# Performance work log

Hardware: AMD Instinct MI355X
Metric: run time of the kernel (lower is better)

Reference implementation:

```python
import jax, jax.numpy as jnp
import numpy as np

B, S, D, H, F, PD = 2, 2048, 768, 12, 3072, 64


def layer_norm(x, w, b, eps=1e-5):
    m = jnp.mean(x, axis=-1, keepdims=True)
    v = jnp.var(x, axis=-1, keepdims=True)
    return (x - m) / jnp.sqrt(v + eps) * w + b


def setup_inputs() -> dict:
    key = jax.random.key(0)
    ks = jax.random.split(key, 8)
    sc = 0.02
    return {
        "x": jax.random.normal(ks[0], (B, S, D), jnp.float32),
        "ln1_w": jnp.ones((D,), jnp.float32),
        "ln1_b": jnp.zeros((D,), jnp.float32),
        "in_proj_w": jax.random.normal(ks[1], (3 * D, D), jnp.float32) * sc,
        "in_proj_b": jnp.zeros((3 * D,), jnp.float32),
        "phase_w": jax.random.normal(ks[2], (PD, D), jnp.float32) * sc,
        "alpha": jnp.float32(0.5),
        "ff_w1": jax.random.normal(ks[3], (F, D), jnp.float32) * sc,
        "ff_b1": jnp.zeros((F,), jnp.float32),
        "ff_w2": jax.random.normal(ks[4], (D, F), jnp.float32) * sc,
        "ff_b2": jnp.zeros((D,), jnp.float32),
        "ln2_w": jnp.ones((D,), jnp.float32),
        "ln2_b": jnp.zeros((D,), jnp.float32),
    }


def reference(x, ln1_w, ln1_b, in_proj_w, in_proj_b, phase_w, alpha,
              ff_w1, ff_b1, ff_w2, ff_b2, ln2_w, ln2_b):
    Dh = D // H
    xn = layer_norm(x, ln1_w, ln1_b)
    # MultiheadAttention with need_weights=True: only the head-averaged
    # softmax(QK^T/sqrt(Dh)) weights are consumed downstream (attn_out is
    # discarded in the original forward, so V/out_proj are dead code).
    qkv = xn @ in_proj_w.T + in_proj_b                       # [B,S,3D]
    q, k, _ = jnp.split(qkv, 3, axis=-1)
    q = q.reshape(B, S, H, Dh) * (1.0 / np.sqrt(Dh)).astype(np.float32)
    k = k.reshape(B, S, H, Dh)
    scores = jnp.einsum('bqhd,bkhd->bhqk', q, k)             # [B,H,S,S]
    attn_w = jax.nn.softmax(scores, axis=-1).mean(axis=1)    # head-avg [B,S,S]
    phase = jnp.tanh(xn @ phase_w.T)                         # [B,S,64]
    phase_coh = (phase @ phase.swapaxes(-2, -1) + 1.0) * 0.5  # [B,S,S]
    blended = jax.nn.softmax(jnp.log(attn_w + 1e-6) + alpha * phase_coh, axis=-1)
    x = x + blended @ xn                                     # enhanced context
    x2 = layer_norm(x, ln2_w, ln2_b)
    h = jax.nn.gelu(x2 @ ff_w1.T + ff_b1, approximate=False)  # exact GELU (torch default)
    ff = h @ ff_w2.T + ff_b2
    return x + ff
```

## Files before the change

### kernel.cpp

```cpp
#include <hip/hip_runtime.h>
#include <math.h>

typedef unsigned short u16;
typedef short bf8 __attribute__((ext_vector_type(8)));
typedef float f4 __attribute__((ext_vector_type(4)));

#define LOG2E 1.44269504088896340736f

__device__ __forceinline__ u16 f2b(float f) {
  union { float f; unsigned int u; } v; v.f = f;
  unsigned int u = v.u;
  return (u16)((u + 0x7FFFu + ((u >> 16) & 1u)) >> 16);
}
__device__ __forceinline__ float b2f(u16 u) {
  union { unsigned int i; float f; } v; v.i = ((unsigned int)u) << 16; return v.f;
}
__device__ __forceinline__ float ex2(float x) {
#if __has_builtin(__builtin_amdgcn_exp2f)
  return __builtin_amdgcn_exp2f(x);
#else
  return exp2f(x);
#endif
}

template <int N>
__device__ __forceinline__ void waitvm() {
  if constexpr (N == 0)      asm volatile("s_waitcnt vmcnt(0)" ::: "memory");
  else if constexpr (N == 4) asm volatile("s_waitcnt vmcnt(4)" ::: "memory");
  else if constexpr (N == 6) asm volatile("s_waitcnt vmcnt(6)" ::: "memory");
  else if constexpr (N == 8) asm volatile("s_waitcnt vmcnt(8)" ::: "memory");
}

#define GLOAD_LDS16(gp, lp)                                                          \
  __builtin_amdgcn_global_load_lds(                                                  \
      reinterpret_cast<const __attribute__((address_space(1))) unsigned int*>(       \
          reinterpret_cast<uintptr_t>(gp)),                                          \
      reinterpret_cast<__attribute__((address_space(3))) unsigned int*>(             \
          reinterpret_cast<uintptr_t>(lp)),                                          \
      16, 0, 0)

template <int ISSUES>
__device__ __forceinline__ void stage_sw(const u16* gbase, long ldg, u16* lds,
                                         int wv, int lane) {
#pragma unroll
  for (int is = 0; is < ISSUES; ++is) {
    const int idx = is * 256 + wv * 64 + lane;
    const int r = idx >> 3, cs = idx & 7;
    const u16* gp = gbase + (long)r * ldg + ((cs ^ (r & 7)) << 3);
    GLOAD_LDS16(gp, (char*)lds + is * 4096 + wv * 1024);
  }
}
__device__ __forceinline__ bf8 frag_sw(const u16* lds, int r, int c) {
  return *(const bf8*)((const char*)lds + r * 128 + ((c ^ (r & 7)) << 4));
}

__global__ __launch_bounds__(256) void conv_bf16_k(const float* __restrict__ in,
                                                   u16* __restrict__ out, int n4) {
  int i = blockIdx.x * 256 + threadIdx.x;
  if (i >= n4) return;
  float4 v = ((const float4*)in)[i];
  union { u16 s[4]; uint2 u; } o;
  o.s[0] = f2b(v.x); o.s[1] = f2b(v.y); o.s[2] = f2b(v.z); o.s[3] = f2b(v.w);
  ((uint2*)out)[i] = o.u;
}

__global__ __launch_bounds__(256) void ln_bf16_k(const float* __restrict__ in,
                                                 const float* __restrict__ w,
                                                 const float* __restrict__ b,
                                                 u16* __restrict__ out) {
  const long row = blockIdx.x;
  const float* xr = in + row * 768;
  const int t = threadIdx.x;
  float v[3];
  float s = 0.f, q = 0.f;
#pragma unroll
  for (int i = 0; i < 3; ++i) {
    v[i] = xr[t + 256 * i];
    s += v[i]; q += v[i] * v[i];
  }
#pragma unroll
  for (int off = 1; off < 64; off <<= 1) { s += __shfl_xor(s, off); q += __shfl_xor(q, off); }
  __shared__ float rs[4], rq[4];
  const int wave = t >> 6, lane = t & 63;
  if (lane == 0) { rs[wave] = s; rq[wave] = q; }
  __syncthreads();
  s = rs[0] + rs[1] + rs[2] + rs[3];
  q = rq[0] + rq[1] + rq[2] + rq[3];
  const float mean = s * (1.0f / 768.0f);
  const float var = q * (1.0f / 768.0f) - mean * mean;
  const float rstd = rsqrtf(var + 1e-5f);
  u16* orow = out + row * 768;
#pragma unroll
  for (int i = 0; i < 3; ++i) {
    const int c = t + 256 * i;
    orow[c] = f2b((v[i] - mean) * rstd * w[c] + b[c]);
  }
}

__global__ __launch_bounds__(256) void transp_k(const u16* __restrict__ in,
                                                u16* __restrict__ out) {
  const int d0 = blockIdx.x * 64, s0 = blockIdx.y * 64;
  __shared__ u16 T[64][72];
  const int t = threadIdx.x;
  {
    const int r = t >> 3, c8 = (t & 7) * 8;
#pragma unroll
    for (int p = 0; p < 2; ++p) {
      const int rr = r + 32 * p;
      *(uint4*)&T[rr][c8] = *(const uint4*)&in[(long)(s0 + rr) * 768 + d0 + c8];
    }
  }
  __syncthreads();
  {
    const int d = t >> 3, s8 = (t & 7) * 8;
#pragma unroll
    for (int p = 0; p < 2; ++p) {
      const int dd = d + 32 * p;
      u16 tmp[8];
#pragma unroll
      for (int e = 0; e < 8; ++e) tmp[e] = T[s8 + e][dd];
      *(uint4*)&out[(long)(d0 + dd) * 4096 + s0 + s8] = *(uint4*)tmp;
    }
  }
}

template <int EPI, int TM>
__global__ __launch_bounds__(256) void mgemm4_k(
    const u16* __restrict__ A, int lda, long sA,
    const u16* __restrict__ B, int ldb, long sB,
    const float* __restrict__ bias,
    const float* __restrict__ res, long sR,
    void* __restrict__ O0, long sO, void* __restrict__ O1, void* __restrict__ O2,
    const int M, const int N, const int K) {
  constexpr int WR = (TM == 128) ? 2 : 1;
  constexpr int WC = 4 / WR;
  constexpr int MR = TM / (WR * 16);
  constexpr int NR = 128 / (WC * 16);
  constexpr int AISS = TM / 32;
  constexpr int BISS = 4;
  constexpr int NS = AISS + BISS;
  constexpr int AW = TM * 64;
  constexpr int BW = 128 * 64;
  __shared__ u16 As[2 * AW];
  __shared__ u16 Bs[2 * BW];
  const int t = threadIdx.x;
  const int wv = t >> 6, lane = t & 63;
  const int lr = lane & 15, lg = lane >> 4;
  const int wr = wv / WC, wc = wv % WC;
  const int wrow0 = wr * (MR * 16), wcol0 = wc * (NR * 16);

  const int gx = gridDim.x;
  const int nwg = gx * gridDim.y;
  const int cpx = nwg >> 3;
  const int flat = blockIdx.x + gx * blockIdx.y;
  const int nf = (flat & 7) * cpx + (flat >> 3);
  const int m0 = (nf / gx) * TM, n0 = (nf % gx) * 128;

  const int bz = blockIdx.z;
  const u16* Ab = A + (long)bz * sA + (long)m0 * lda;
  const u16* Bb = B + (long)bz * sB + (long)n0 * ldb;
  const long zR = (long)bz * sR, zO = (long)bz * sO;

  const u16* ga[AISS];
  const u16* gb[BISS];
#pragma unroll
  for (int is = 0; is < AISS; ++is) {
    const int idx = is * 256 + wv * 64 + lane;
    const int r = idx >> 3, cs = idx & 7;
    ga[is] = Ab + (long)r * lda + ((cs ^ (r & 7)) << 3);
  }
#pragma unroll
  for (int is = 0; is < BISS; ++is) {
    const int idx = is * 256 + wv * 64 + lane;
    const int r = idx >> 3, cs = idx & 7;
    gb[is] = Bb + (long)r * ldb + ((cs ^ (r & 7)) << 3);
  }

  int offA[2][MR], offB[2][NR];
#pragma unroll
  for (int i = 0; i < MR; ++i) {
    const int r = wrow0 + i * 16 + lr;
    offA[0][i] = r * 128 + ((lg ^ (r & 7)) << 4);
    offA[1][i] = r * 128 + (((4 + lg) ^ (r & 7)) << 4);
  }
#pragma unroll
  for (int j = 0; j < NR; ++j) {
    const int r = wcol0 + j * 16 + lr;
    offB[0][j] = r * 128 + ((lg ^ (r & 7)) << 4);
    offB[1][j] = r * 128 + (((4 + lg) ^ (r & 7)) << 4);
  }

  f4 acc[MR][NR];
  const f4 fz = {0.f, 0.f, 0.f, 0.f};
#pragma unroll
  for (int i = 0; i < MR; ++i)
#pragma unroll
    for (int j = 0; j < NR; ++j) acc[i][j] = fz;

#pragma unroll
  for (int is = 0; is < AISS; ++is) {
    GLOAD_LDS16(ga[is], (char*)As + is * 4096 + wv * 1024);
    ga[is] += 64;
  }
#pragma unroll
  for (int is = 0; is < BISS; ++is) {
    GLOAD_LDS16(gb[is], (char*)Bs + is * 4096 + wv * 1024);
    gb[is] += 64;
  }

  const int NT = K >> 6;
  int cur = 0;
  for (int kt = 0; kt < NT; ++kt) {
    if (kt + 1 < NT) {
      char* bufA = (char*)(As + (cur ^ 1) * AW);
      char* bufB = (char*)(Bs + (cur ^ 1) * BW);
#pragma unroll
      for (int is = 0; is < AISS; ++is) {
        GLOAD_LDS16(ga[is], bufA + is * 4096 + wv * 1024);
        ga[is] += 64;
      }
#pragma unroll
      for (int is = 0; is < BISS; ++is) {
        GLOAD_LDS16(gb[is], bufB + is * 4096 + wv * 1024);
        gb[is] += 64;
      }
      waitvm<NS>();
    } else {
      waitvm<0>();
    }
    __builtin_amdgcn_s_barrier();
    const char* a = (const char*)(As + cur * AW);
    const char* b = (const char*)(Bs + cur * BW);
    bf8 af[2][MR], bf[2][NR];
#pragma unroll
    for (int s = 0; s < 2; ++s) {
#pragma unroll
      for (int i = 0; i < MR; ++i) af[s][i] = *(const bf8*)(a + offA[s][i]);
#pragma unroll
      for (int j = 0; j < NR; ++j) bf[s][j] = *(const bf8*)(b + offB[s][j]);
    }
#pragma unroll
    for (int s = 0; s < 2; ++s)
#pragma unroll
      for (int i = 0; i < MR; ++i)
#pragma unroll
        for (int j = 0; j < NR; ++j)
          acc[i][j] = __builtin_amdgcn_mfma_f32_16x16x32_bf16(af[s][i], bf[s][j], acc[i][j], 0, 0, 0);
    __builtin_amdgcn_s_barrier();
    cur ^= 1;
  }

#pragma unroll
  for (int i = 0; i < MR; ++i) {
    const int gr0 = m0 + wrow0 + i * 16 + lg * 4;
#pragma unroll
    for (int j = 0; j < NR; ++j) {
      const int gc = n0 + wcol0 + j * 16 + lr;
#pragma unroll
      for (int r = 0; r < 4; ++r) {
        const long row = gr0 + r;
        float v = acc[i][j][r];
        if (EPI == 0) {
          if (gc < 1536) {
            v += bias[gc];
            if (gc < 768) ((u16*)O0)[row * 768 + gc] = f2b(v * (0.125f * LOG2E));
            else          ((u16*)O1)[row * 768 + gc - 768] = f2b(v);
          } else if (gc < 1600) {
            ((u16*)O2)[row * 64 + gc - 1536] = f2b(tanhf(v));
          }
        } else if (EPI == 3) {
          v += bias[gc];
          ((u16*)O0)[row * N + gc] = f2b(0.5f * v * (1.0f + erff(v * 0.70710678118654752f)));
        } else if (EPI == 4) {
          ((float*)O0)[row * N + gc] = v + bias[gc] + res[row * N + gc];
        } else {
          const float sc = bias[(long)bz * M + row];
          ((float*)O0)[zO + row * N + gc] = v * sc + res[zR + row * N + gc];
        }
      }
    }
  }
}

__global__ __launch_bounds__(256) void attn_stats3(const u16* __restrict__ qb,
                                                   const u16* __restrict__ kb,
                                                   float* __restrict__ Ms_g) {
  const int qt = blockIdx.x, h = blockIdx.y, b = blockIdx.z;
  const int t = threadIdx.x, wv = t >> 6, lane = t & 63;
  const int lr = lane & 15, lg = lane >> 4;
  __shared__ u16 Qs[64 * 64];
  __shared__ u16 Ks[2][128 * 64];
  __shared__ float zbuf[4][64];
  const long q0 = (long)b * 2048 + qt * 64;
  const long kbase = ((long)b * 2048) * 768 + h * 64;
  stage_sw<2>(qb + q0 * 768 + h * 64, 768, Qs, wv, lane);
  stage_sw<4>(kb + kbase, 768, Ks[0], wv, lane);
  waitvm<4>();
  __builtin_amdgcn_s_barrier();

  bf8 aq[4][2];
#pragma unroll
  for (int i = 0; i < 4; ++i)
#pragma unroll
    for (int kk = 0; kk < 2; ++kk)
      aq[i][kk] = frag_sw(Qs, i * 16 + lr, kk * 4 + lg);

  float zp[4][4];
#pragma unroll
  for (int i = 0; i < 4; ++i)
#pragma unroll
    for (int r = 0; r < 4; ++r) zp[i][r] = 0.f;

  const f4 fz = {0.f, 0.f, 0.f, 0.f};
  int cur = 0;
  for (int kt = 0; kt < 16; ++kt) {
    if (kt < 15) {
      stage_sw<4>(kb + kbase + (long)(kt + 1) * 128 * 768, 768, Ks[cur ^ 1], wv, lane);
      waitvm<4>();
    } else {
      waitvm<0>();
    }
    __builtin_amdgcn_s_barrier();
#pragma unroll
    for (int j = 0; j < 2; ++j) {
      const int krow = wv * 32 + j * 16 + lr;
      const bf8 b0 = frag_sw(Ks[cur], krow, lg);
      const bf8 b1 = frag_sw(Ks[cur], krow, 4 + lg);
#pragma unroll
      for (int i = 0; i < 4; ++i) {
        f4 s = fz;
        s = __builtin_amdgcn_mfma_f32_16x16x32_bf16(aq[i][0], b0, s, 0, 0, 0);
        s = __builtin_amdgcn_mfma_f32_16x16x32_bf16(aq[i][1], b1, s, 0, 0, 0);
#pragma unroll
        for (int r = 0; r < 4; ++r) zp[i][r] += ex2(s[r]);
      }
    }
    __builtin_amdgcn_s_barrier();
    cur ^= 1;
  }
#pragma unroll
  for (int i = 0; i < 4; ++i)
#pragma unroll
    for (int r = 0; r < 4; ++r) {
      float z = zp[i][r];
      z += __shfl_xor(z, 1); z += __shfl_xor(z, 2);
      z += __shfl_xor(z, 4); z += __shfl_xor(z, 8);
      zp[i][r] = z;
    }
  if (lr == 0) {
#pragma unroll
    for (int i = 0; i < 4; ++i)
#pragma unroll
      for (int r = 0; r < 4; ++r)
        zbuf[wv][i * 16 + lg * 4 + r] = zp[i][r];
  }
  __syncthreads();
  if (t < 64) {
    const float Z = zbuf[0][t] + zbuf[1][t] + zbuf[2][t] + zbuf[3][t];
    Ms_g[((long)(b * 12 + h)) * 2048 + qt * 64 + t] = log2f(12.0f * Z);
  }
}

__global__ __launch_bounds__(256) void blendpre5(const u16* __restrict__ qb,
                                                 const u16* __restrict__ kb,
                                                 const u16* __restrict__ ph,
                                                 const float* __restrict__ Ms_g,
                                                 const float* __restrict__ alpha_p,
                                                 u16* __restrict__ eb) {
  const int kt = blockIdx.x, qt = blockIdx.y, b = blockIdx.z;
  const int t = threadIdx.x, wv = t >> 6, lane = t & 63;
  const int lr = lane & 15, lg = lane >> 4;
  const int wr = wv >> 1, wc = wv & 1;
  const int q0 = qt * 128, k0 = kt * 128;
  __shared__ u16 Qs[2][128 * 64];
  __shared__ u16 Ks[2][128 * 64];
  __shared__ float Ms[12][128];
  for (int idx = t; idx < 1536; idx += 256)
    Ms[idx >> 7][idx & 127] = Ms_g[((long)(b * 12 + (idx >> 7))) * 2048 + q0 + (idx & 127)];
  asm volatile("s_waitcnt vmcnt(0) lgkmcnt(0)" ::: "memory");
  __builtin_amdgcn_s_barrier();
  const float a2 = alpha_p[0] * 0.5f * LOG2E;

  f4 acc[4][4];
  const f4 fz = {0.f, 0.f, 0.f, 0.f};
#pragma unroll
  for (int i = 0; i < 4; ++i)
#pragma unroll
    for (int j = 0; j < 4; ++j) acc[i][j] = fz;

  const long qrow0 = (long)b * 2048 + q0;
  const long krow0 = (long)b * 2048 + k0;

  stage_sw<4>(qb + qrow0 * 768, 768, Qs[0], wv, lane);
  stage_sw<4>(kb + krow0 * 768, 768, Ks[0], wv, lane);

  int cur = 0;
  for (int h = 0; h < 12; ++h) {
    if (h < 11) {
      stage_sw<4>(qb + qrow0 * 768 + (h + 1) * 64, 768, Qs[cur ^ 1], wv, lane);
      stage_sw<4>(kb + krow0 * 768 + (h + 1) * 64, 768, Ks[cur ^ 1], wv, lane);
      waitvm<8>();
    } else {
      waitvm<0>();
    }
    __builtin_amdgcn_s_barrier();
    bf8 aq0[4], aq1[4], bk0[4], bk1[4];
#pragma unroll
    for (int i = 0; i < 4; ++i) {
      aq0[i] = frag_sw(Qs[cur], wr * 64 + i * 16 + lr, lg);
      aq1[i] = frag_sw(Qs[cur], wr * 64 + i * 16 + lr, 4 + lg);
    }
#pragma unroll
    for (int j = 0; j < 4; ++j) {
      bk0[j] = frag_sw(Ks[cur], wc * 64 + j * 16 + lr, lg);
      bk1[j] = frag_sw(Ks[cur], wc * 64 + j * 16 + lr, 4 + lg);
    }
#pragma unroll
    for (int i = 0; i < 4; ++i) {
      const f4 mv = *(const f4*)&Ms[h][wr * 64 + i * 16 + lg * 4];
      const f4 cin = fz - mv;
#pragma unroll
      for (int j = 0; j < 4; ++j) {
        f4 s = __builtin_amdgcn_mfma_f32_16x16x32_bf16(aq0[i], bk0[j], cin, 0, 0, 0);
        s = __builtin_amdgcn_mfma_f32_16x16x32_bf16(aq1[i], bk1[j], s, 0, 0, 0);
#pragma unroll
        for (int r = 0; r < 4; ++r) acc[i][j][r] += ex2(s[r]);
      }
    }
    __builtin_amdgcn_s_barrier();
    cur ^= 1;
  }

#pragma unroll
  for (int i = 0; i < 4; ++i) {
    const u16* pa = ph + (qrow0 + wr * 64 + i * 16 + lr) * 64;
    const bf8 pa0 = *(const bf8*)(pa + lg * 8);
    const bf8 pa1 = *(const bf8*)(pa + 32 + lg * 8);
#pragma unroll
    for (int j = 0; j < 4; ++j) {
      const u16* pb = ph + (krow0 + wc * 64 + j * 16 + lr) * 64;
      const bf8 pb0 = *(const bf8*)(pb + lg * 8);
      const bf8 pb1 = *(const bf8*)(pb + 32 + lg * 8);
      f4 coh = fz;
      coh = __builtin_amdgcn_mfma_f32_16x16x32_bf16(pa0, pb0, coh, 0, 0, 0);
      coh = __builtin_amdgcn_mfma_f32_16x16x32_bf16(pa1, pb1, coh, 0, 0, 0);
#pragma unroll
      for (int r = 0; r < 4; ++r) {
        const long row = qrow0 + wr * 64 + i * 16 + lg * 4 + r;
        const int col = k0 + wc * 64 + j * 16 + lr;
        const float e = (acc[i][j][r] + 1e-6f) * ex2(a2 * (coh[r] + 1.0f));
        eb[row * 2048 + col] = f2b(e);
      }
    }
  }
}

__global__ __launch_bounds__(256) void rowsum_k(const u16* __restrict__ eb,
                                                float* __restrict__ rinv) {
  const long row = blockIdx.x;
  const int t = threadIdx.x, wv = t >> 6, lane = t & 63;
  const uint4 pv = ((const uint4*)(eb + row * 2048))[t];
  float s = b2f(pv.x & 0xffff) + b2f(pv.x >> 16) + b2f(pv.y & 0xffff) + b2f(pv.y >> 16) +
            b2f(pv.z & 0xffff) + b2f(pv.z >> 16) + b2f(pv.w & 0xffff) + b2f(pv.w >> 16);
#pragma unroll
  for (int off = 1; off < 64; off <<= 1) s += __shfl_xor(s, off);
  __shared__ float red[4];
  if (lane == 0) red[wv] = s;
  __syncthreads();
  if (t == 0) rinv[row] = 1.0f / (red[0] + red[1] + red[2] + red[3]);
}

extern "C" void kernel_launch(void* const* d_in, const int* in_sizes, int n_in,
                              void* d_out, int out_size, void* d_ws, size_t ws_size,
                              hipStream_t stream) {
  (void)in_sizes; (void)n_in; (void)out_size; (void)ws_size;
  const float* x         = (const float*)d_in[0];
  const float* ln1_w     = (const float*)d_in[1];
  const float* ln1_b     = (const float*)d_in[2];
  const float* in_proj_w = (const float*)d_in[3];
  const float* in_proj_b = (const float*)d_in[4];
  const float* phase_w   = (const float*)d_in[5];
  const float* alpha_p   = (const float*)d_in[6];
  const float* ff_w1     = (const float*)d_in[7];
  const float* ff_b1     = (const float*)d_in[8];
  const float* ff_w2     = (const float*)d_in[9];
  const float* ff_b2     = (const float*)d_in[10];
  const float* ln2_w     = (const float*)d_in[11];
  const float* ln2_b     = (const float*)d_in[12];
  float* out = (float*)d_out;

  char* w = (char*)d_ws;
  u16*   xn_b  = (u16*)w;            w += 6291456;
  u16*   xnT_b = (u16*)w;            w += 6291456;
  u16*   ph_b  = (u16*)w;            w += 524288;
  float* Ms_g  = (float*)w;          w += 196608;
  float* xmid  = (float*)w;          w += 12582912;
  char* big = w;
  u16* q_b  = (u16*)big;
  u16* k_b  = (u16*)(big + 6291456);
  u16* eb_b = (u16*)(big + 12582912);
  char* tail = big + 12582912 + 16777216;
  u16* wcat_b = (u16*)tail;
  float* rinv = (float*)(tail + 2555904);
  u16* h_b  = (u16*)big;
  char* wtail = tail + 16777216;
  u16* wff1_b = (u16*)wtail;
  u16* wff2_b = (u16*)(wtail + 4718592);
  u16* x2n_b = xn_b;

  conv_bf16_k<<<(1536 * 768 / 4 + 255) / 256, 256, 0, stream>>>(in_proj_w, wcat_b, 1536 * 768 / 4);
  conv_bf16_k<<<(64 * 768 / 4 + 255) / 256, 256, 0, stream>>>(phase_w, wcat_b + 1536 * 768, 64 * 768 / 4);
  conv_bf16_k<<<(3072 * 768 / 4 + 255) / 256, 256, 0, stream>>>(ff_w1, wff1_b, 3072 * 768 / 4);
  conv_bf16_k<<<(768 * 3072 / 4 + 255) / 256, 256, 0, stream>>>(ff_w2, wff2_b, 768 * 3072 / 4);

  ln_bf16_k<<<4096, 256, 0, stream>>>(x, ln1_w, ln1_b, xn_b);

  mgemm4_k<0, 128><<<dim3(13, 32, 1), 256, 0, stream>>>(
      xn_b, 768, 0, wcat_b, 768, 0, in_proj_b, nullptr, 0,
      q_b, 0, k_b, ph_b, 4096, 1664, 768);

  transp_k<<<dim3(12, 64), 256, 0, stream>>>(xn_b, xnT_b);

  attn_stats3<<<dim3(32, 12, 2), 256, 0, stream>>>(q_b, k_b, Ms_g);

  blendpre5<<<dim3(16, 16, 2), 256, 0, stream>>>(q_b, k_b, ph_b, Ms_g, alpha_p, eb_b);

  rowsum_k<<<4096, 256, 0, stream>>>(eb_b, rinv);

  mgemm4_k<5, 64><<<dim3(6, 32, 2), 256, 0, stream>>>(
      eb_b, 2048, 2048L * 2048, xnT_b, 4096, 2048, rinv, x, 2048L * 768,
      xmid, 2048L * 768, nullptr, nullptr, 2048, 768, 2048);

  ln_bf16_k<<<4096, 256, 0, stream>>>(xmid, ln2_w, ln2_b, x2n_b);

  mgemm4_k<3, 128><<<dim3(24, 32, 1), 256, 0, stream>>>(
      x2n_b, 768, 0, wff1_b, 768, 0, ff_b1, nullptr, 0,
      h_b, 0, nullptr, nullptr, 4096, 3072, 768);

  mgemm4_k<4, 64><<<dim3(6, 64, 1), 256, 0, stream>>>(
      h_b, 3072, 0, wff2_b, 3072, 0, ff_b2, xmid, 0,
      out, 0, nullptr, nullptr, 4096, 768, 3072);
}
```

Before: 213.5 us.

## Fuse row sums into blend kernel, group GEMM tiles, use fast tanh/GELU

Row sums of the blended exponentials are accumulated in the blend kernel with shuffles and atomics, removing the separate rowsum pass over the large score buffer. The sum buffer is zeroed in the transpose kernel, and the reciprocal moves into the GEMM epilogue. GEMM tile mapping is grouped in column bands of eight for cache locality. Exact erf GELU and tanhf are replaced by exp2/rcp-based tanh approximations, which changes numerics slightly, and the atomics make the summation order nondeterministic.

```diff
diff --git a/kernel.cpp b/kernel.cpp
--- a/kernel.cpp
+++ b/kernel.cpp
@@ -21,6 +21,20 @@
 #else
   return exp2f(x);
 #endif
+}
+__device__ __forceinline__ float rcp_f(float x) {
+#if __has_builtin(__builtin_amdgcn_rcpf)
+  return __builtin_amdgcn_rcpf(x);
+#else
+  return 1.0f / x;
+#endif
+}
+__device__ __forceinline__ float fast_tanh(float y) {
+  return 1.0f - 2.0f * rcp_f(ex2(y * (2.0f * LOG2E)) + 1.0f);
+}
+__device__ __forceinline__ float fast_gelu(float v) {
+  const float u = v * (0.79788456080286536f + 0.03567740814f * v * v);
+  return 0.5f * v * (1.0f + fast_tanh(u));
 }
 
 template <int N>
@@ -98,10 +112,15 @@
 }
 
 __global__ __launch_bounds__(256) void transp_k(const u16* __restrict__ in,
-                                                u16* __restrict__ out) {
+                                                u16* __restrict__ out,
+                                                float* __restrict__ rsum) {
   const int d0 = blockIdx.x * 64, s0 = blockIdx.y * 64;
+  const int t = threadIdx.x;
+  {
+    const int bid = blockIdx.x + 12 * blockIdx.y;
+    if (bid < 16) rsum[bid * 256 + t] = 0.f;
+  }
   __shared__ u16 T[64][72];
-  const int t = threadIdx.x;
   {
     const int r = t >> 3, c8 = (t & 7) * 8;
 #pragma unroll
@@ -125,7 +144,7 @@
 }
 
 template <int EPI, int TM>
-__global__ __launch_bounds__(256) void mgemm4_k(
+__global__ __launch_bounds__(256) void mgemm5_k(
     const u16* __restrict__ A, int lda, long sA,
     const u16* __restrict__ B, int ldb, long sB,
     const float* __restrict__ bias,
@@ -149,12 +168,19 @@
   const int wr = wv / WC, wc = wv % WC;
   const int wrow0 = wr * (MR * 16), wcol0 = wc * (NR * 16);
 
-  const int gx = gridDim.x;
-  const int nwg = gx * gridDim.y;
+  const int gx = gridDim.x, gy = gridDim.y;
+  const int nwg = gx * gy;
   const int cpx = nwg >> 3;
   const int flat = blockIdx.x + gx * blockIdx.y;
   const int nf = (flat & 7) * cpx + (flat >> 3);
-  const int m0 = (nf / gx) * TM, n0 = (nf % gx) * 128;
+  constexpr int G = 8;
+  const int npg = G * gy;
+  const int grp = nf / npg;
+  const int firstn = grp * G;
+  const int gsz = (gx - firstn < G) ? (gx - firstn) : G;
+  const int rem = nf - grp * npg;
+  const int m0 = (rem / gsz) * TM;
+  const int n0 = (firstn + rem % gsz) * 128;
 
   const int bz = blockIdx.z;
   const u16* Ab = A + (long)bz * sA + (long)m0 * lda;
@@ -266,15 +292,14 @@
             if (gc < 768) ((u16*)O0)[row * 768 + gc] = f2b(v * (0.125f * LOG2E));
             else          ((u16*)O1)[row * 768 + gc - 768] = f2b(v);
           } else if (gc < 1600) {
-            ((u16*)O2)[row * 64 + gc - 1536] = f2b(tanhf(v));
+            ((u16*)O2)[row * 64 + gc - 1536] = f2b(fast_tanh(v));
           }
         } else if (EPI == 3) {
-          v += bias[gc];
-          ((u16*)O0)[row * N + gc] = f2b(0.5f * v * (1.0f + erff(v * 0.70710678118654752f)));
+          ((u16*)O0)[row * N + gc] = f2b(fast_gelu(v + bias[gc]));
         } else if (EPI == 4) {
           ((float*)O0)[row * N + gc] = v + bias[gc] + res[row * N + gc];
         } else {
-          const float sc = bias[(long)bz * M + row];
+          const float sc = rcp_f(bias[(long)bz * M + row]);
           ((float*)O0)[zO + row * N + gc] = v * sc + res[zR + row * N + gc];
         }
       }
@@ -361,12 +386,13 @@
   }
 }
 
-__global__ __launch_bounds__(256) void blendpre5(const u16* __restrict__ qb,
+__global__ __launch_bounds__(256) void blendpre6(const u16* __restrict__ qb,
                                                  const u16* __restrict__ kb,
                                                  const u16* __restrict__ ph,
                                                  const float* __restrict__ Ms_g,
                                                  const float* __restrict__ alpha_p,
-                                                 u16* __restrict__ eb) {
+                                                 u16* __restrict__ eb,
+                                                 float* __restrict__ rsum) {
   const int kt = blockIdx.x, qt = blockIdx.y, b = blockIdx.z;
   const int t = threadIdx.x, wv = t >> 6, lane = t & 63;
   const int lr = lane & 15, lg = lane >> 4;
@@ -431,6 +457,12 @@
     cur ^= 1;
   }
 
+  float rs[4][4];
+#pragma unroll
+  for (int i = 0; i < 4; ++i)
+#pragma unroll
+    for (int r = 0; r < 4; ++r) rs[i][r] = 0.f;
+
 #pragma unroll
   for (int i = 0; i < 4; ++i) {
     const u16* pa = ph + (qrow0 + wr * 64 + i * 16 + lr) * 64;
@@ -450,24 +482,20 @@
         const int col = k0 + wc * 64 + j * 16 + lr;
         const float e = (acc[i][j][r] + 1e-6f) * ex2(a2 * (coh[r] + 1.0f));
         eb[row * 2048 + col] = f2b(e);
+        rs[i][r] += e;
       }
     }
   }
-}
-
-__global__ __launch_bounds__(256) void rowsum_k(const u16* __restrict__ eb,
-                                                float* __restrict__ rinv) {
-  const long row = blockIdx.x;
-  const int t = threadIdx.x, wv = t >> 6, lane = t & 63;
-  const uint4 pv = ((const uint4*)(eb + row * 2048))[t];
-  float s = b2f(pv.x & 0xffff) + b2f(pv.x >> 16) + b2f(pv.y & 0xffff) + b2f(pv.y >> 16) +
-            b2f(pv.z & 0xffff) + b2f(pv.z >> 16) + b2f(pv.w & 0xffff) + b2f(pv.w >> 16);
-#pragma unroll
-  for (int off = 1; off < 64; off <<= 1) s += __shfl_xor(s, off);
-  __shared__ float red[4];
-  if (lane == 0) red[wv] = s;
-  __syncthreads();
-  if (t == 0) rinv[row] = 1.0f / (red[0] + red[1] + red[2] + red[3]);
+#pragma unroll
+  for (int i = 0; i < 4; ++i)
+#pragma unroll
+    for (int r = 0; r < 4; ++r) {
+      float v = rs[i][r];
+      v += __shfl_xor(v, 1); v += __shfl_xor(v, 2);
+      v += __shfl_xor(v, 4); v += __shfl_xor(v, 8);
+      if (lr == 0)
+        atomicAdd(&rsum[qrow0 + wr * 64 + i * 16 + lg * 4 + r], v);
+    }
 }
 
 extern "C" void kernel_launch(void* const* d_in, const int* in_sizes, int n_in,
@@ -501,7 +529,7 @@
   u16* eb_b = (u16*)(big + 12582912);
   char* tail = big + 12582912 + 16777216;
   u16* wcat_b = (u16*)tail;
-  float* rinv = (float*)(tail + 2555904);
+  float* rsum = (float*)(tail + 2555904);
   u16* h_b  = (u16*)big;
   char* wtail = tail + 16777216;
   u16* wff1_b = (u16*)wtail;
@@ -515,29 +543,27 @@
 
   ln_bf16_k<<<4096, 256, 0, stream>>>(x, ln1_w, ln1_b, xn_b);
 
-  mgemm4_k<0, 128><<<dim3(13, 32, 1), 256, 0, stream>>>(
+  mgemm5_k<0, 128><<<dim3(13, 32, 1), 256, 0, stream>>>(
       xn_b, 768, 0, wcat_b, 768, 0, in_proj_b, nullptr, 0,
       q_b, 0, k_b, ph_b, 4096, 1664, 768);
 
-  transp_k<<<dim3(12, 64), 256, 0, stream>>>(xn_b, xnT_b);
+  transp_k<<<dim3(12, 64), 256, 0, stream>>>(xn_b, xnT_b, rsum);
 
   attn_stats3<<<dim3(32, 12, 2), 256, 0, stream>>>(q_b, k_b, Ms_g);
 
-  blendpre5<<<dim3(16, 16, 2), 256, 0, stream>>>(q_b, k_b, ph_b, Ms_g, alpha_p, eb_b);
-
-  rowsum_k<<<4096, 256, 0, stream>>>(eb_b, rinv);
-
-  mgemm4_k<5, 64><<<dim3(6, 32, 2), 256, 0, stream>>>(
-      eb_b, 2048, 2048L * 2048, xnT_b, 4096, 2048, rinv, x, 2048L * 768,
+  blendpre6<<<dim3(16, 16, 2), 256, 0, stream>>>(q_b, k_b, ph_b, Ms_g, alpha_p, eb_b, rsum);
+
+  mgemm5_k<5, 64><<<dim3(6, 32, 2), 256, 0, stream>>>(
+      eb_b, 2048, 2048L * 2048, xnT_b, 4096, 2048, rsum, x, 2048L * 768,
       xmid, 2048L * 768, nullptr, nullptr, 2048, 768, 2048);
 
   ln_bf16_k<<<4096, 256, 0, stream>>>(xmid, ln2_w, ln2_b, x2n_b);
 
-  mgemm4_k<3, 128><<<dim3(24, 32, 1), 256, 0, stream>>>(
+  mgemm5_k<3, 128><<<dim3(24, 32, 1), 256, 0, stream>>>(
       x2n_b, 768, 0, wff1_b, 768, 0, ff_b1, nullptr, 0,
       h_b, 0, nullptr, nullptr, 4096, 3072, 768);
 
-  mgemm4_k<4, 64><<<dim3(6, 64, 1), 256, 0, stream>>>(
+  mgemm5_k<4, 64><<<dim3(6, 64, 1), 256, 0, stream>>>(
       h_b, 3072, 0, wff2_b, 3072, 0, ff_b2, xmid, 0,
       out, 0, nullptr, nullptr, 4096, 768, 3072);
 }
```

New measurement: 197.8 us. -7.3%, faster.
